# Performance work log

Measured on AMD Instinct MI355X. Metric: run time of the kernel, lower is better.

## Reference

```python
import jax, jax.numpy as jnp
import numpy as np

# Elman RNN (SRNN). Dropout is treated as identity (eval/inference mode),
# since the reference baseline must be deterministic.

def setup_inputs() -> dict:
    key = jax.random.key(0)
    k1, k2, k3, k4 = jax.random.split(key, 4)
    B, S, I, H = 32, 2048, 256, 256
    x = jax.random.normal(k1, (B, S, I), dtype=jnp.float32)
    Wx_w = jax.random.normal(k2, (H, I), dtype=jnp.float32) * (1.0 / np.sqrt(I))
    Wx_b = jax.random.normal(k3, (H,), dtype=jnp.float32) * 0.01
    Wh_w = jax.random.normal(k4, (H, H), dtype=jnp.float32) * (1.0 / np.sqrt(H))
    return {"x": x, "Wx_w": Wx_w, "Wx_b": Wx_b, "Wh_w": Wh_w}


def reference(x, Wx_w, Wx_b, Wh_w):
    B, S, I = x.shape
    H = Wx_w.shape[0]
    # Precompute input projection for all timesteps in one batched GEMM: [B,S,H]
    xw = jnp.einsum('bsi,hi->bsh', x, Wx_w) + Wx_b
    xw_t = jnp.swapaxes(xw, 0, 1)  # [S,B,H] for scan over time

    def step(h, xw_step):
        h_new = jnp.tanh(xw_step + h @ Wh_w.T)  # [B,H]
        return h_new, h_new

    h0 = jnp.zeros((B, H), dtype=x.dtype)
    h_last, outs = jax.lax.scan(step, h0, xw_t)  # outs: [S,B,H]
    outputs = jnp.swapaxes(outs, 0, 1)  # [B,S,H]
    return outputs, h_last
```

## Files before the change

kernel.cpp:

```cpp
#include <hip/hip_runtime.h>

#define B 32
#define S 2048
#define I 256
#define H 256

typedef _Float16 h2 __attribute__((ext_vector_type(2)));

__device__ __forceinline__ float fdot2(h2 a, h2 b, float c) {
#if __has_builtin(__builtin_amdgcn_fdot2)
    return __builtin_amdgcn_fdot2(a, b, c, false);
#else
    return fmaf((float)a[1], (float)b[1], fmaf((float)a[0], (float)b[0], c));
#endif
}

__device__ __forceinline__ void lds_barrier() {
    __asm__ __volatile__("" ::: "memory");
    __builtin_amdgcn_s_waitcnt(0xC07F);
    __builtin_amdgcn_s_barrier();
    __asm__ __volatile__("" ::: "memory");
}

__device__ __forceinline__ float fast_tanh(float x) {
#if __has_builtin(__builtin_amdgcn_exp2f) && __has_builtin(__builtin_amdgcn_rcpf)
    float e = __builtin_amdgcn_exp2f(x * 2.8853900818f);
    float r = __builtin_amdgcn_rcpf(e + 1.0f);
    return fmaf(-2.0f, r, 1.0f);
#else
    float e = __expf(2.0f * x);
    return 1.0f - __fdividef(2.0f, e + 1.0f);
#endif
}

__device__ __forceinline__ float dpp_xor1(float x) {
    return __builtin_bit_cast(float, __builtin_amdgcn_mov_dpp(
        __builtin_bit_cast(int, x), 0xB1, 0xF, 0xF, false));
}
__device__ __forceinline__ float dpp_xor2(float x) {
    return __builtin_bit_cast(float, __builtin_amdgcn_mov_dpp(
        __builtin_bit_cast(int, x), 0x4E, 0xF, 0xF, false));
}

#define TM 128
#define TN 128
#define TK 32
#define LDP (TM + 4)

__global__ __launch_bounds__(256) void phase1_gemm(
    const float* __restrict__ x, const float* __restrict__ Wxw,
    const float* __restrict__ Wxb, float* __restrict__ out)
{
    __shared__ __align__(16) float As[TK][LDP];
    __shared__ __align__(16) float Bs[TK][LDP];

    const int t  = threadIdx.x;
    const int tn = t & 15, tm = t >> 4;
    const int m0 = blockIdx.x * TM;
    const int n0 = blockIdx.y * TN;

    float acc[8][8] = {};
    float bias[8];
#pragma unroll
    for (int j = 0; j < 4; ++j) {
        bias[j]     = Wxb[n0 + 4 * tn + j];
        bias[4 + j] = Wxb[n0 + 64 + 4 * tn + j];
    }

    const int lr = t >> 3;
    const int lc = t & 7;

    float4 va[4], vb[4];
#pragma unroll
    for (int hh = 0; hh < 4; ++hh) {
        const int m = lr + 32 * hh;
        va[hh] = *(const float4*)(x   + (size_t)(m0 + m) * I + 4 * lc);
        vb[hh] = *(const float4*)(Wxw + (size_t)(n0 + m) * I + 4 * lc);
    }

    for (int kt = 0; kt < I; kt += TK) {
#pragma unroll
        for (int hh = 0; hh < 4; ++hh) {
            const int m = lr + 32 * hh;
            float4 v = va[hh];
            As[4 * lc + 0][m] = v.x; As[4 * lc + 1][m] = v.y;
            As[4 * lc + 2][m] = v.z; As[4 * lc + 3][m] = v.w;
            float4 wv = vb[hh];
            Bs[4 * lc + 0][m] = wv.x; Bs[4 * lc + 1][m] = wv.y;
            Bs[4 * lc + 2][m] = wv.z; Bs[4 * lc + 3][m] = wv.w;
        }
        lds_barrier();
        if (kt + TK < I) {
#pragma unroll
            for (int hh = 0; hh < 4; ++hh) {
                const int m = lr + 32 * hh;
                va[hh] = *(const float4*)(x   + (size_t)(m0 + m) * I + kt + TK + 4 * lc);
                vb[hh] = *(const float4*)(Wxw + (size_t)(n0 + m) * I + kt + TK + 4 * lc);
            }
        }
#pragma unroll
        for (int k = 0; k < TK; ++k) {
            float4 a0 = *(const float4*)&As[k][4 * tm];
            float4 a1 = *(const float4*)&As[k][4 * tm + 64];
            float4 b0 = *(const float4*)&Bs[k][4 * tn];
            float4 b1 = *(const float4*)&Bs[k][4 * tn + 64];
            float av[8] = {a0.x, a0.y, a0.z, a0.w, a1.x, a1.y, a1.z, a1.w};
            float bv[8] = {b0.x, b0.y, b0.z, b0.w, b1.x, b1.y, b1.z, b1.w};
#pragma unroll
            for (int i2 = 0; i2 < 8; ++i2)
#pragma unroll
                for (int j = 0; j < 8; ++j)
                    acc[i2][j] = fmaf(av[i2], bv[j], acc[i2][j]);
        }
        lds_barrier();
    }
#pragma unroll
    for (int hi = 0; hi < 2; ++hi) {
#pragma unroll
        for (int i2 = 0; i2 < 4; ++i2) {
            const int r = m0 + 64 * hi + 4 * tm + i2;
            float4 v0 = { acc[4 * hi + i2][0] + bias[0], acc[4 * hi + i2][1] + bias[1],
                          acc[4 * hi + i2][2] + bias[2], acc[4 * hi + i2][3] + bias[3] };
            float4 v1 = { acc[4 * hi + i2][4] + bias[4], acc[4 * hi + i2][5] + bias[5],
                          acc[4 * hi + i2][6] + bias[6], acc[4 * hi + i2][7] + bias[7] };
            *(float4*)(out + (size_t)r * H + n0 + 4 * tn)      = v0;
            *(float4*)(out + (size_t)r * H + n0 + 64 + 4 * tn) = v1;
        }
    }
}

__global__ __launch_bounds__(256, 1) void phase2_rnn(
    const float* __restrict__ Whw, float* __restrict__ out)
{
    __shared__ __align__(16) _Float16 hsh[2][4][72];

    const int b = blockIdx.x;
    const int t = threadIdx.x;
    const int w = t >> 6;
    const int l = t & 63;
    const int j = l >> 2;
    const int q = l & 3;

    h2 wreg[4][32];
#pragma unroll
    for (int i = 0; i < 4; ++i) {
        const float4* wp =
            (const float4*)(Whw + (size_t)(64 * w + 4 * j + (q ^ i)) * H + 64 * q);
#pragma unroll
        for (int m = 0; m < 16; ++m) {
            float4 f = wp[m];
            wreg[i][2 * m]     = h2{(_Float16)f.x, (_Float16)f.y};
            wreg[i][2 * m + 1] = h2{(_Float16)f.z, (_Float16)f.w};
        }
    }
#pragma unroll
    for (int i = 0; i < 4; ++i)
#pragma unroll
        for (int m = 0; m < 32; ++m) {
            unsigned tmp = __builtin_bit_cast(unsigned, wreg[i][m]);
            __asm__("" : "+v"(tmp));
            wreg[i][m] = __builtin_bit_cast(h2, tmp);
        }

    hsh[0][w][l] = (_Float16)0.0f;
    __syncthreads();

    float* outb = out + (size_t)b * S * H + t;
    float*       op = outb;
    const float* lp = outb + 2 * (size_t)H;
    float xw0 = outb[0], xw1 = outb[(size_t)H];

    float hv = 0.f;
#pragma unroll 2
    for (int s = 0; s < S; ++s) {
        const int p = s & 1;
        float xwn = lp[0]; lp += H;

        const uint4* hp = (const uint4*)&hsh[p][q][0];
        float acc0 = 0.f, acc1 = 0.f, acc2 = 0.f, acc3 = 0.f;
#pragma unroll
        for (int u = 0; u < 8; ++u) {
            uint4 v = hp[u];
            h2 q0 = __builtin_bit_cast(h2, v.x);
            h2 q1 = __builtin_bit_cast(h2, v.y);
            h2 q2 = __builtin_bit_cast(h2, v.z);
            h2 q3 = __builtin_bit_cast(h2, v.w);
            acc0 = fdot2(wreg[0][4 * u + 0], q0, acc0);
            acc0 = fdot2(wreg[0][4 * u + 1], q1, acc0);
            acc0 = fdot2(wreg[0][4 * u + 2], q2, acc0);
            acc0 = fdot2(wreg[0][4 * u + 3], q3, acc0);
            acc1 = fdot2(wreg[1][4 * u + 0], q0, acc1);
            acc1 = fdot2(wreg[1][4 * u + 1], q1, acc1);
            acc1 = fdot2(wreg[1][4 * u + 2], q2, acc1);
            acc1 = fdot2(wreg[1][4 * u + 3], q3, acc1);
            acc2 = fdot2(wreg[2][4 * u + 0], q0, acc2);
            acc2 = fdot2(wreg[2][4 * u + 1], q1, acc2);
            acc2 = fdot2(wreg[2][4 * u + 2], q2, acc2);
            acc2 = fdot2(wreg[2][4 * u + 3], q3, acc2);
            acc3 = fdot2(wreg[3][4 * u + 0], q0, acc3);
            acc3 = fdot2(wreg[3][4 * u + 1], q1, acc3);
            acc3 = fdot2(wreg[3][4 * u + 2], q2, acc3);
            acc3 = fdot2(wreg[3][4 * u + 3], q3, acc3);
        }

        float Sa  = acc0 + dpp_xor1(acc1);
        float Sb  = acc2 + dpp_xor1(acc3);
        float sum = Sa + dpp_xor2(Sb);

        hv = fast_tanh(xw0 + sum);
        hsh[p ^ 1][w][l] = (_Float16)hv;
        op[0] = hv; op += H;

        lds_barrier();

        xw0 = xw1; xw1 = xwn;
    }
    out[(size_t)B * S * H + (size_t)b * H + t] = hv;
}

extern "C" void kernel_launch(void* const* d_in, const int* in_sizes, int n_in,
                              void* d_out, int out_size, void* d_ws, size_t ws_size,
                              hipStream_t stream) {
    const float* x   = (const float*)d_in[0];
    const float* Wxw = (const float*)d_in[1];
    const float* Wxb = (const float*)d_in[2];
    const float* Whw = (const float*)d_in[3];
    float* out = (float*)d_out;

    dim3 g1(B * S / TM, H / TN);
    phase1_gemm<<<g1, 256, 0, stream>>>(x, Wxw, Wxb, out);
    phase2_rnn<<<B, 256, 0, stream>>>(Whw, out);
}
```

Before: 1.029 ms.

## Fuse GEMM and RNN into one persistent kernel with flag-based overlap

```diff
diff --git a/kernel.cpp b/kernel.cpp
--- a/kernel.cpp
+++ b/kernel.cpp
@@ -4,6 +4,11 @@
 #define S 2048
 #define I 256
 #define H 256
+
+#define NWORK  224
+#define NRNN   32
+#define NTILE  1024
+#define NFLAG  512
 
 typedef _Float16 h2 __attribute__((ext_vector_type(2)));
 
@@ -42,33 +47,37 @@
         __builtin_bit_cast(int, x), 0x4E, 0xF, 0xF, false));
 }
 
+__device__ __forceinline__ void wait_flag(const int* f) {
+    long long t0 = __builtin_amdgcn_s_memrealtime();
+    while (__hip_atomic_load(f, __ATOMIC_ACQUIRE, __HIP_MEMORY_SCOPE_AGENT) != 2) {
+        __builtin_amdgcn_s_sleep(8);
+        if (__builtin_amdgcn_s_memrealtime() - t0 > 25000000LL) break;
+    }
+}
+
+__global__ void zero_flags(int* flags) { flags[threadIdx.x] = 0; }
+
 #define TM 128
 #define TN 128
 #define TK 32
 #define LDP (TM + 4)
 
-__global__ __launch_bounds__(256) void phase1_gemm(
+__device__ __forceinline__ void gemm_tile(
     const float* __restrict__ x, const float* __restrict__ Wxw,
-    const float* __restrict__ Wxb, float* __restrict__ out)
-{
-    __shared__ __align__(16) float As[TK][LDP];
-    __shared__ __align__(16) float Bs[TK][LDP];
-
-    const int t  = threadIdx.x;
+    const float* __restrict__ Wxb, float* __restrict__ out,
+    float (*As)[LDP], float (*Bs)[LDP], int t, int m0, int n0)
+{
+    const int lr = t >> 3;
+    const int lc = t & 7;
     const int tn = t & 15, tm = t >> 4;
-    const int m0 = blockIdx.x * TM;
-    const int n0 = blockIdx.y * TN;
 
     float acc[8][8] = {};
     float bias[8];
 #pragma unroll
-    for (int j = 0; j < 4; ++j) {
-        bias[j]     = Wxb[n0 + 4 * tn + j];
-        bias[4 + j] = Wxb[n0 + 64 + 4 * tn + j];
-    }
-
-    const int lr = t >> 3;
-    const int lc = t & 7;
+    for (int jj = 0; jj < 4; ++jj) {
+        bias[jj]     = Wxb[n0 + 4 * tn + jj];
+        bias[4 + jj] = Wxb[n0 + 64 + 4 * tn + jj];
+    }
 
     float4 va[4], vb[4];
 #pragma unroll
@@ -109,8 +118,8 @@
 #pragma unroll
             for (int i2 = 0; i2 < 8; ++i2)
 #pragma unroll
-                for (int j = 0; j < 8; ++j)
-                    acc[i2][j] = fmaf(av[i2], bv[j], acc[i2][j]);
+                for (int jj = 0; jj < 8; ++jj)
+                    acc[i2][jj] = fmaf(av[i2], bv[jj], acc[i2][jj]);
         }
         lds_barrier();
     }
@@ -129,13 +138,10 @@
     }
 }
 
-__global__ __launch_bounds__(256, 1) void phase2_rnn(
-    const float* __restrict__ Whw, float* __restrict__ out)
-{
-    __shared__ __align__(16) _Float16 hsh[2][4][72];
-
-    const int b = blockIdx.x;
-    const int t = threadIdx.x;
+__device__ __forceinline__ void rnn_body(
+    const float* __restrict__ Whw, float* __restrict__ out,
+    _Float16 (*hsh)[4][72], int b, int t, const int* flags)
+{
     const int w = t >> 6;
     const int l = t & 63;
     const int j = l >> 2;
@@ -165,6 +171,11 @@
     hsh[0][w][l] = (_Float16)0.0f;
     __syncthreads();
 
+    if (flags) {
+        if (t == 0) wait_flag(flags + 0);
+        __syncthreads();
+    }
+
     float* outb = out + (size_t)b * S * H + t;
     float*       op = outb;
     const float* lp = outb + 2 * (size_t)H;
@@ -174,6 +185,10 @@
 #pragma unroll 2
     for (int s = 0; s < S; ++s) {
         const int p = s & 1;
+        if (flags && ((s + 2) & 127) == 0 && s + 2 < S) {
+            if (t == 0) wait_flag(flags + ((s + 2) >> 7));
+            __syncthreads();
+        }
         float xwn = lp[0]; lp += H;
 
         const uint4* hp = (const uint4*)&hsh[p][q][0];
@@ -218,6 +233,53 @@
     out[(size_t)B * S * H + (size_t)b * H + t] = hv;
 }
 
+__global__ __launch_bounds__(256, 1) void fused_srnn(
+    const float* __restrict__ x, const float* __restrict__ Wxw,
+    const float* __restrict__ Wxb, const float* __restrict__ Whw,
+    float* __restrict__ out, int* __restrict__ flags)
+{
+    __shared__ __align__(16) float As[TK][LDP];
+    __shared__ __align__(16) float Bs[TK][LDP];
+    __shared__ __align__(16) _Float16 hsh[2][4][72];
+
+    const int bid = blockIdx.x;
+    const int t   = threadIdx.x;
+
+    if (bid < NWORK) {
+        for (int tau = bid; tau < NTILE; tau += NWORK) {
+            const int st = tau >> 6;
+            const int bb = (tau >> 1) & 31;
+            const int nt = tau & 1;
+            gemm_tile(x, Wxw, Wxb, out, As, Bs, t,
+                      bb * S + st * TM, nt * TN);
+            __threadfence();
+            __syncthreads();
+            if (t == 0)
+                __hip_atomic_fetch_add(&flags[bb * 16 + st], 1,
+                                       __ATOMIC_RELEASE, __HIP_MEMORY_SCOPE_AGENT);
+        }
+        return;
+    }
+    rnn_body(Whw, out, hsh, bid - NWORK, t, flags + (bid - NWORK) * 16);
+}
+
+__global__ __launch_bounds__(256) void phase1_gemm(
+    const float* __restrict__ x, const float* __restrict__ Wxw,
+    const float* __restrict__ Wxb, float* __restrict__ out)
+{
+    __shared__ __align__(16) float As[TK][LDP];
+    __shared__ __align__(16) float Bs[TK][LDP];
+    gemm_tile(x, Wxw, Wxb, out, As, Bs, threadIdx.x,
+              blockIdx.x * TM, blockIdx.y * TN);
+}
+
+__global__ __launch_bounds__(256, 1) void phase2_rnn(
+    const float* __restrict__ Whw, float* __restrict__ out)
+{
+    __shared__ __align__(16) _Float16 hsh[2][4][72];
+    rnn_body(Whw, out, hsh, blockIdx.x, threadIdx.x, nullptr);
+}
+
 extern "C" void kernel_launch(void* const* d_in, const int* in_sizes, int n_in,
                               void* d_out, int out_size, void* d_ws, size_t ws_size,
                               hipStream_t stream) {
@@ -227,7 +289,13 @@
     const float* Whw = (const float*)d_in[3];
     float* out = (float*)d_out;
 
-    dim3 g1(B * S / TM, H / TN);
-    phase1_gemm<<<g1, 256, 0, stream>>>(x, Wxw, Wxb, out);
-    phase2_rnn<<<B, 256, 0, stream>>>(Whw, out);
-}
+    if (d_ws != nullptr && ws_size >= NFLAG * sizeof(int)) {
+        int* flags = (int*)d_ws;
+        zero_flags<<<1, NFLAG, 0, stream>>>(flags);
+        fused_srnn<<<NWORK + NRNN, 256, 0, stream>>>(x, Wxw, Wxb, Whw, out, flags);
+    } else {
+        dim3 g1(B * S / TM, H / TN);
+        phase1_gemm<<<g1, 256, 0, stream>>>(x, Wxw, Wxb, out);
+        phase2_rnn<<<B, 256, 0, stream>>>(Whw, out);
+    }
+}
```

Measured after the change: 1.079 ms. +4.8%, slower.
